# Kernel tuning notes

Hardware: AMD Instinct MI355X
Metric: run time of the kernel (lower is better)

Reference implementation:

```python
import jax, jax.numpy as jnp
import numpy as np

N_ITER = 100
EPS = 1e-12


def _corr(x, k):
    # x: [C,H,W], k: [kh,kw]; per-channel 'same' cross-correlation, zero padding
    C = x.shape[0]
    kern = jnp.broadcast_to(k, (C, 1) + k.shape)
    return jax.lax.conv_general_dilated(
        x[None], kern, window_strides=(1, 1), padding='SAME',
        feature_group_count=C,
        dimension_numbers=('NCHW', 'OIHW', 'NCHW'))[0]


def _corr_t(x, k):
    # adjoint of zero-padded 'same' correlation = correlation with flipped kernel
    return _corr(x, k[::-1, ::-1])


def _A(x, kernel, reg_kernels, w2):
    # A x = K^T K x + sum_i w_i^2 R_i^T R_i x
    out = _corr_t(_corr(x, kernel), kernel)
    for i in range(reg_kernels.shape[0]):  # small fixed number of reg kernels
        rk = reg_kernels[i]
        out = out + w2[i] * _corr_t(_corr(x, rk), rk)
    return out


def setup_inputs() -> dict:
    key = jax.random.key(0)
    k1, k2, k3, k4 = jax.random.split(key, 4)
    image = jax.random.uniform(k1, (3, 768, 768), dtype=jnp.float32)
    kernel = jax.random.uniform(k2, (15, 15), dtype=jnp.float32)
    kernel = kernel / jnp.sum(kernel)  # normalized blur PSF
    reg_kernels = jax.random.normal(k3, (2, 5, 5), dtype=jnp.float32)
    reg_kernel_weights = jax.random.uniform(
        k4, (2,), dtype=jnp.float32, minval=1e-6, maxval=1.0)
    return {'image': image, 'kernel': kernel, 'reg_kernels': reg_kernels,
            'reg_kernel_weights': reg_kernel_weights}


def reference(image, kernel, reg_kernels, reg_kernel_weights):
    w2 = reg_kernel_weights ** 2
    # CG init: x0 = image, b = image, solve A x = K^T b
    KTb = _corr_t(image, kernel)
    r0 = KTb - _A(image, kernel, reg_kernels, w2)
    xrp0 = jnp.stack([image, r0, r0])  # [3, C, H, W]: x, r, p

    def body(xrp, _):
        x, r, p = xrp[0], xrp[1], xrp[2]
        Ap = _A(p, kernel, reg_kernels, w2)
        rtr = jnp.sum(r * r, axis=(1, 2), keepdims=True)      # per-channel [C,1,1]
        ptAp = jnp.sum(p * Ap, axis=(1, 2), keepdims=True)
        alpha = rtr / (ptAp + EPS)
        x_new = x + alpha * p
        r_new = r - alpha * Ap
        beta = jnp.sum(r_new * r_new, axis=(1, 2), keepdims=True) / (rtr + EPS)
        p_new = r_new + beta * p
        return jnp.stack([x_new, r_new, p_new]), None

    xrp, _ = jax.lax.scan(jax.checkpoint(body), xrp0, None, length=N_ITER)
    return xrp
```

## Files before the change

### kernel.cpp

```cpp
#include <hip/hip_runtime.h>

#define EPS 1e-12f

constexpr int H = 768, W = 768, C = 3;
constexpr int HW = H * W;
constexpr int CHW = C * HW;

constexpr int NSLOT = 16;
constexpr int SSTR = 16;
constexpr int SCALSZ = NSLOT * SSTR;

constexpr int SPW = 100, SPH = 60;
constexpr int S0W = 84,  S0H = 46;
constexpr int S1W = 76,  S1H = 36;
constexpr int UBUF = SPH * SPW;

constexpr int IPW = 92, IPH = 60;

__device__ __forceinline__ float block_reduce_256(float v, float* redbuf) {
    #pragma unroll
    for (int off = 32; off > 0; off >>= 1) v += __shfl_down(v, off, 64);
    const int tid = threadIdx.x;
    if ((tid & 63) == 0) redbuf[tid >> 6] = v;
    __syncthreads();
    return redbuf[0] + redbuf[1] + redbuf[2] + redbuf[3];
}

__device__ __forceinline__ float sum_slots(const float* base, int c) {
    float s = 0.f;
    #pragma unroll
    for (int k = 0; k < NSLOT; ++k) s += base[k * SSTR + c];
    return s;
}

__global__ void tap_prep_k(const float* __restrict__ k15, const float* __restrict__ rks,
                           const float* __restrict__ rw, float* __restrict__ taps) {
    const int tid = threadIdx.x;
    if (tid < 240) {
        const int i = tid >> 4, j = tid & 15;
        taps[tid]       = (j < 15) ? k15[i * 15 + j] : 0.f;
        taps[240 + tid] = (j < 15) ? k15[(14 - i) * 15 + (14 - j)] : 0.f;
    }
    if (tid < 80) {
        const int kk = tid / 40, rem = tid % 40, i = rem >> 3, j = rem & 7;
        taps[480 + tid] = (j < 5) ? rks[kk * 25 + i * 5 + j] : 0.f;
        taps[560 + tid] = (j < 5) ? rks[kk * 25 + (4 - i) * 5 + (4 - j)] : 0.f;
    }
    const float w20 = rw[0] * rw[0], w21 = rw[1] * rw[1];
    for (int t = tid; t < 29 * 36; t += 256) {
        const int uy = t / 36, ux = t - uy * 36;
        float s = 0.f;
        if (ux < 29) {
            const int dy = uy - 14, dx = ux - 14;
            for (int sy = 0; sy < 15; ++sy) {
                const int ty = sy + dy;
                if ((unsigned)ty >= 15u) continue;
                for (int sx = 0; sx < 15; ++sx) {
                    const int tx = sx + dx;
                    if ((unsigned)tx < 15u) s += k15[sy * 15 + sx] * k15[ty * 15 + tx];
                }
            }
            if (dy >= -4 && dy <= 4 && dx >= -4 && dx <= 4) {
                float q0 = 0.f, q1 = 0.f;
                for (int sy = 0; sy < 5; ++sy) {
                    const int ty = sy + dy;
                    if ((unsigned)ty >= 5u) continue;
                    for (int sx = 0; sx < 5; ++sx) {
                        const int tx = sx + dx;
                        if ((unsigned)tx >= 5u) continue;
                        q0 += rks[sy * 5 + sx] * rks[ty * 5 + tx];
                        q1 += rks[25 + sy * 5 + sx] * rks[25 + ty * 5 + tx];
                    }
                }
                s += w20 * q0 + w21 * q1;
            }
        }
        taps[640 + t] = s;
    }
}

template <bool WRITEP>
__global__ __launch_bounds__(256) void interiorA_k(
    const float* __restrict__ pprev, const float* __restrict__ rvec,
    const float* __restrict__ tk,
    float* __restrict__ Ap, float* __restrict__ outP,
    const float* __restrict__ bnum, const float* __restrict__ bden,
    float* __restrict__ red)
{
    __shared__ __align__(16) float pe[IPH * IPW];
    __shared__ float redbuf[4];
    const int c = blockIdx.z;
    const int bx = 64 + blockIdx.x * 64, by = 32 + blockIdx.y * 32;
    const int tid = threadIdx.x;
    const float beta = sum_slots(bnum, c) / (sum_slots(bden, c) + EPS);
    const float* pC = pprev + c * HW;
    const float* rC = rvec + c * HW;
    const int gy0 = by - 14, gx0 = bx - 14;

    for (int t = tid; t < IPH * IPW; t += 256) {
        const int ly = t / IPW, lx = t - ly * IPW;
        const int g = (gy0 + ly) * W + gx0 + lx;
        pe[t] = fmaf(beta, pC[g], rC[g]);
    }
    __syncthreads();

    const int ox = (tid & 15) << 2;
    const int o0 = (tid >> 4) << 1;

    float a0[4], a1[4];
    #pragma unroll
    for (int k = 0; k < 4; ++k) { a0[k] = 0.f; a1[k] = 0.f; }

    {
        const float* rp = pe + o0 * IPW + ox;
        float seg[32];
        #pragma unroll
        for (int q = 0; q < 8; ++q) *(float4*)(seg + 4 * q) = *(const float4*)(rp + 4 * q);
        #pragma unroll
        for (int j = 0; j < 29; ++j) {
            const float kv = tk[j];
            #pragma unroll
            for (int k = 0; k < 4; ++k) a0[k] = fmaf(seg[j + k], kv, a0[k]);
        }
    }
    #pragma unroll 1
    for (int d = 1; d <= 28; ++d) {
        const float* rp = pe + (o0 + d) * IPW + ox;
        float seg[32];
        #pragma unroll
        for (int q = 0; q < 8; ++q) *(float4*)(seg + 4 * q) = *(const float4*)(rp + 4 * q);
        const float* kr0 = tk + d * 36;
        const float* kr1 = kr0 - 36;
        #pragma unroll
        for (int j = 0; j < 29; ++j) {
            const float kv0 = kr0[j], kv1 = kr1[j];
            #pragma unroll
            for (int k = 0; k < 4; ++k) {
                a0[k] = fmaf(seg[j + k], kv0, a0[k]);
                a1[k] = fmaf(seg[j + k], kv1, a1[k]);
            }
        }
    }
    {
        const float* rp = pe + (o0 + 29) * IPW + ox;
        float seg[32];
        #pragma unroll
        for (int q = 0; q < 8; ++q) *(float4*)(seg + 4 * q) = *(const float4*)(rp + 4 * q);
        const float* kr1 = tk + 28 * 36;
        #pragma unroll
        for (int j = 0; j < 29; ++j) {
            const float kv = kr1[j];
            #pragma unroll
            for (int k = 0; k < 4; ++k) a1[k] = fmaf(seg[j + k], kv, a1[k]);
        }
    }

    const int gbase = c * HW + (by + o0) * W + bx + ox;
    const float* c0p = pe + (o0 + 14) * IPW + ox + 14;
    const float* c1p = c0p + IPW;
    *(float4*)(Ap + gbase)     = make_float4(a0[0], a0[1], a0[2], a0[3]);
    *(float4*)(Ap + gbase + W) = make_float4(a1[0], a1[1], a1[2], a1[3]);
    float local = 0.f;
    #pragma unroll
    for (int k = 0; k < 4; ++k) local += c0p[k] * a0[k] + c1p[k] * a1[k];
    if (WRITEP) {
        *(float4*)(outP + gbase)     = make_float4(c0p[0], c0p[1], c0p[2], c0p[3]);
        *(float4*)(outP + gbase + W) = make_float4(c1p[0], c1p[1], c1p[2], c1p[3]);
    }
    const float tot = block_reduce_256(local, redbuf);
    if (tid == 0) {
        const int bid = blockIdx.y * gridDim.x + blockIdx.x;
        atomicAdd(red + (bid & (NSLOT - 1)) * SSTR + c, tot);
    }
}

template <int MODE, bool REMAP>
__global__ __launch_bounds__(256) void fusedA_k(
    const float* __restrict__ in, const float* __restrict__ rvec,
    const float* __restrict__ taps, const float* __restrict__ rw,
    float* __restrict__ Ap, float* __restrict__ outR,
    float* __restrict__ outP, float* __restrict__ outX,
    const float* __restrict__ bnum, const float* __restrict__ bden,
    float* __restrict__ red)
{
    __shared__ __align__(16) float ub[UBUF];
    __shared__ __align__(16) float st1[S1H * S1W];
    __shared__ __align__(16) float st2[S1H * S1W];
    __shared__ float redbuf[4];

    const float* kt   = taps;
    const float* ktf  = taps + 240;
    const float* rkt  = taps + 480;
    const float* rktf = taps + 560;

    int tbx, tby;
    if (REMAP) {
        const int e = blockIdx.x;
        if (e < 12)      { tbx = e;      tby = 0; }
        else if (e < 24) { tbx = e - 12; tby = 23; }
        else if (e < 46) { tbx = 0;      tby = 1 + (e - 24); }
        else             { tbx = 11;     tby = 1 + (e - 46); }
    } else { tbx = blockIdx.x; tby = blockIdx.y; }

    const int c = blockIdx.z;
    const int bx = tbx * 64, by = tby * 32;
    const int tid = threadIdx.x;
    const float* inC = in + c * HW;

    float beta = 0.f;
    if (MODE == 2) beta = sum_slots(bnum, c) / (sum_slots(bden, c) + EPS);

    for (int t = tid; t < SPH * 96; t += 256) {
        const int ly = t / 96, lx = t - ly * 96;
        const int gy = by - 14 + ly, gx = bx - 14 + lx;
        float v = 0.f;
        if ((unsigned)gy < (unsigned)H && (unsigned)gx < (unsigned)W) {
            const int g = gy * W + gx;
            v = inC[g];
            if (MODE == 2) v = rvec[c * HW + g] + beta * v;
        }
        ub[ly * SPW + lx] = v;
    }
    __syncthreads();

    const int oy = tid >> 3;
    const int ox = (tid & 7) << 3;

    {
        const int s0 = tid, s1 = tid + 256;
        const int row0 = s0 / 9, c0 = (s0 - row0 * 9) << 3;
        const int row1 = s1 / 9, c1 = (s1 - row1 * 9) << 3;
        const bool v1 = (s1 < 324);
        float b0[8], c0a[8], b1[8], c1a[8];
        #pragma unroll
        for (int k = 0; k < 8; ++k) { b0[k] = 0.f; c0a[k] = 0.f; b1[k] = 0.f; c1a[k] = 0.f; }

        float4 kb0 = *(const float4*)(rkt + 0), kb1 = *(const float4*)(rkt + 4);
        float4 kc0 = *(const float4*)(rkt + 40), kc1 = *(const float4*)(rkt + 44);
        #pragma unroll 1
        for (int i = 0; i < 5; ++i) {
            const int ip = (i < 4) ? i + 1 : 4;
            float4 nb0 = *(const float4*)(rkt + ip * 8),      nb1 = *(const float4*)(rkt + ip * 8 + 4);
            float4 nc0 = *(const float4*)(rkt + 40 + ip * 8), nc1 = *(const float4*)(rkt + 40 + ip * 8 + 4);
            float kb[8], kc[8];
            *(float4*)(kb) = kb0; *(float4*)(kb + 4) = kb1;
            *(float4*)(kc) = kc0; *(float4*)(kc + 4) = kc1;
            {
                const float* rp = ub + (row0 + 10 + i) * SPW + c0 + 8;
                float seg[16];
                #pragma unroll
                for (int q = 0; q < 4; ++q) *(float4*)(seg + 4 * q) = *(const float4*)(rp + 4 * q);
                #pragma unroll
                for (int j = 0; j < 5; ++j)
                    #pragma unroll
                    for (int k = 0; k < 8; ++k) {
                        b0[k]  = fmaf(seg[j + k + 2], kb[j], b0[k]);
                        c0a[k] = fmaf(seg[j + k + 2], kc[j], c0a[k]);
                    }
            }
            if (v1) {
                const float* rp = ub + (row1 + 10 + i) * SPW + c1 + 8;
                float seg[16];
                #pragma unroll
                for (int q = 0; q < 4; ++q) *(float4*)(seg + 4 * q) = *(const float4*)(rp + 4 * q);
                #pragma unroll
                for (int j = 0; j < 5; ++j)
                    #pragma unroll
                    for (int k = 0; k < 8; ++k) {
                        b1[k]  = fmaf(seg[j + k + 2], kb[j], b1[k]);
                        c1a[k] = fmaf(seg[j + k + 2], kc[j], c1a[k]);
                    }
            }
            kb0 = nb0; kb1 = nb1; kc0 = nc0; kc1 = nc1;
        }
        {
            const int gy = by - 2 + row0, gxb = bx - 2 + c0;
            #pragma unroll
            for (int k = 0; k < 8; ++k) {
                const bool bad = ((unsigned)gy >= (unsigned)H) || ((unsigned)(gxb + k) >= (unsigned)W);
                if (bad) { b0[k] = 0.f; c0a[k] = 0.f; }
            }
            float* o1 = st1 + row0 * S1W + c0;
            float* o2 = st2 + row0 * S1W + c0;
            *(float4*)(o1)     = make_float4(b0[0], b0[1], b0[2], b0[3]);
            *(float4*)(o1 + 4) = make_float4(b0[4], b0[5], b0[6], b0[7]);
            *(float4*)(o2)     = make_float4(c0a[0], c0a[1], c0a[2], c0a[3]);
            *(float4*)(o2 + 4) = make_float4(c0a[4], c0a[5], c0a[6], c0a[7]);
        }
        if (v1) {
            const int gy = by - 2 + row1, gxb = bx - 2 + c1;
            #pragma unroll
            for (int k = 0; k < 8; ++k) {
                const bool bad = ((unsigned)gy >= (unsigned)H) || ((unsigned)(gxb + k) >= (unsigned)W);
                if (bad) { b1[k] = 0.f; c1a[k] = 0.f; }
            }
            float* o1 = st1 + row1 * S1W + c1;
            float* o2 = st2 + row1 * S1W + c1;
            *(float4*)(o1)     = make_float4(b1[0], b1[1], b1[2], b1[3]);
            *(float4*)(o1 + 4) = make_float4(b1[4], b1[5], b1[6], b1[7]);
            *(float4*)(o2)     = make_float4(c1a[0], c1a[1], c1a[2], c1a[3]);
            *(float4*)(o2 + 4) = make_float4(c1a[4], c1a[5], c1a[6], c1a[7]);
        }
    }

    float pctr[8];
    {
        const float* ctr = ub + (oy + 14) * SPW + ox + 14;
        #pragma unroll
        for (int k = 0; k < 8; ++k) pctr[k] = ctr[k];
    }

    float vimg[8];
    if (MODE == 0) {
        #pragma unroll
        for (int k = 0; k < 8; ++k) vimg[k] = 0.f;
        #pragma unroll 1
        for (int i = 0; i < 15; ++i) {
            const float* rowp = ub + (oy + 7 + i) * SPW + ox + 4;
            float seg[28];
            #pragma unroll
            for (int q = 0; q < 7; ++q) *(float4*)(seg + 4 * q) = *(const float4*)(rowp + 4 * q);
            float kv[16];
            #pragma unroll
            for (int q = 0; q < 4; ++q) *(float4*)(kv + 4 * q) = *(const float4*)(ktf + i * 16 + 4 * q);
            #pragma unroll
            for (int j = 0; j < 15; ++j)
                #pragma unroll
                for (int k = 0; k < 8; ++k) vimg[k] = fmaf(seg[j + k + 3], kv[j], vimg[k]);
        }
    }

    const int s0 = tid, s1 = tid + 256;
    const int row0 = s0 / 10, ca0 = (s0 - row0 * 10) << 3;
    const int row1 = s1 / 10, ca1 = (s1 - row1 * 10) << 3;
    const bool av1 = (s1 < 460);
    float a0[8], a1[8];
    #pragma unroll
    for (int k = 0; k < 8; ++k) { a0[k] = 0.f; a1[k] = 0.f; }
    {
        float4 k0 = *(const float4*)(kt + 0), k1 = *(const float4*)(kt + 4);
        float4 k2 = *(const float4*)(kt + 8), k3 = *(const float4*)(kt + 12);
        #pragma unroll 1
        for (int i = 0; i < 15; ++i) {
            const int ip = (i < 14) ? i + 1 : 14;
            float4 n0 = *(const float4*)(kt + ip * 16),     n1 = *(const float4*)(kt + ip * 16 + 4);
            float4 n2 = *(const float4*)(kt + ip * 16 + 8), n3 = *(const float4*)(kt + ip * 16 + 12);
            float kv[16];
            *(float4*)(kv) = k0; *(float4*)(kv + 4) = k1;
            *(float4*)(kv + 8) = k2; *(float4*)(kv + 12) = k3;
            {
                const float* rp = ub + (row0 + i) * SPW + ca0;
                float seg[24];
                #pragma unroll
                for (int q = 0; q < 6; ++q) *(float4*)(seg + 4 * q) = *(const float4*)(rp + 4 * q);
                #pragma unroll
                for (int j = 0; j < 15; ++j)
                    #pragma unroll
                    for (int k = 0; k < 8; ++k) a0[k] = fmaf(seg[j + k], kv[j], a0[k]);
            }
            if (av1) {
                const float* rp = ub + (row1 + i) * SPW + ca1;
                float seg[24];
                #pragma unroll
                for (int q = 0; q < 6; ++q) *(float4*)(seg + 4 * q) = *(const float4*)(rp + 4 * q);
                #pragma unroll
                for (int j = 0; j < 15; ++j)
                    #pragma unroll
                    for (int k = 0; k < 8; ++k) a1[k] = fmaf(seg[j + k], kv[j], a1[k]);
            }
            k0 = n0; k1 = n1; k2 = n2; k3 = n3;
        }
    }
    {
        const int gy = by - 7 + row0, gxb = bx - 7 + ca0;
        #pragma unroll
        for (int k = 0; k < 8; ++k)
            if (((unsigned)gy >= (unsigned)H) || ((unsigned)(gxb + k) >= (unsigned)W)) a0[k] = 0.f;
    }
    if (av1) {
        const int gy = by - 7 + row1, gxb = bx - 7 + ca1;
        #pragma unroll
        for (int k = 0; k < 8; ++k)
            if (((unsigned)gy >= (unsigned)H) || ((unsigned)(gxb + k) >= (unsigned)W)) a1[k] = 0.f;
    }

    __syncthreads();

    {
        float* o = ub + row0 * S0W + ca0;
        *(float4*)(o)     = make_float4(a0[0], a0[1], a0[2], a0[3]);
        *(float4*)(o + 4) = make_float4(a0[4], a0[5], a0[6], a0[7]);
    }
    if (av1) {
        float* o = ub + row1 * S0W + ca1;
        *(float4*)(o)     = make_float4(a1[0], a1[1], a1[2], a1[3]);
        *(float4*)(o + 4) = make_float4(a1[4], a1[5], a1[6], a1[7]);
    }
    __syncthreads();

    float acc[8];
    #pragma unroll
    for (int k = 0; k < 8; ++k) acc[k] = 0.f;
    {
        float4 k0 = *(const float4*)(ktf + 0), k1 = *(const float4*)(ktf + 4);
        float4 k2 = *(const float4*)(ktf + 8), k3 = *(const float4*)(ktf + 12);
        #pragma unroll 1
        for (int i = 0; i < 15; ++i) {
            const int ip = (i < 14) ? i + 1 : 14;
            float4 n0 = *(const float4*)(ktf + ip * 16),     n1 = *(const float4*)(ktf + ip * 16 + 4);
            float4 n2 = *(const float4*)(ktf + ip * 16 + 8), n3 = *(const float4*)(ktf + ip * 16 + 12);
            float kv[16];
            *(float4*)(kv) = k0; *(float4*)(kv + 4) = k1;
            *(float4*)(kv + 8) = k2; *(float4*)(kv + 12) = k3;
            const float* rp = ub + (oy + i) * S0W + ox;
            float seg[24];
            #pragma unroll
            for (int q = 0; q < 6; ++q) *(float4*)(seg + 4 * q) = *(const float4*)(rp + 4 * q);
            #pragma unroll
            for (int j = 0; j < 15; ++j)
                #pragma unroll
                for (int k = 0; k < 8; ++k) acc[k] = fmaf(seg[j + k], kv[j], acc[k]);
            k0 = n0; k1 = n1; k2 = n2; k3 = n3;
        }
    }

    float accB[8], accC[8];
    #pragma unroll
    for (int k = 0; k < 8; ++k) { accB[k] = 0.f; accC[k] = 0.f; }
    {
        float4 kb0 = *(const float4*)(rktf + 0), kb1 = *(const float4*)(rktf + 4);
        float4 kc0 = *(const float4*)(rktf + 40), kc1 = *(const float4*)(rktf + 44);
        #pragma unroll 1
        for (int i = 0; i < 5; ++i) {
            const int ip = (i < 4) ? i + 1 : 4;
            float4 nb0 = *(const float4*)(rktf + ip * 8),      nb1 = *(const float4*)(rktf + ip * 8 + 4);
            float4 nc0 = *(const float4*)(rktf + 40 + ip * 8), nc1 = *(const float4*)(rktf + 40 + ip * 8 + 4);
            float kb[8], kc[8];
            *(float4*)(kb) = kb0; *(float4*)(kb + 4) = kb1;
            *(float4*)(kc) = kc0; *(float4*)(kc + 4) = kc1;
            const float* r1p = st1 + (oy + i) * S1W + ox;
            const float* r2p = st2 + (oy + i) * S1W + ox;
            float sA[12], sB[12];
            #pragma unroll
            for (int q = 0; q < 3; ++q) *(float4*)(sA + 4 * q) = *(const float4*)(r1p + 4 * q);
            #pragma unroll
            for (int q = 0; q < 3; ++q) *(float4*)(sB + 4 * q) = *(const float4*)(r2p + 4 * q);
            #pragma unroll
            for (int j = 0; j < 5; ++j)
                #pragma unroll
                for (int k = 0; k < 8; ++k) {
                    accB[k] = fmaf(sA[j + k], kb[j], accB[k]);
                    accC[k] = fmaf(sB[j + k], kc[j], accC[k]);
                }
            kb0 = nb0; kb1 = nb1; kc0 = nc0; kc1 = nc1;
        }
    }

    const float w0 = rw[0], w1 = rw[1];
    const float w02 = w0 * w0, w12 = w1 * w1;
    float v[8];
    #pragma unroll
    for (int k = 0; k < 8; ++k) v[k] = acc[k] + w02 * accB[k] + w12 * accC[k];

    const int g = c * HW + (by + oy) * W + bx + ox;
    float local = 0.f;
    if (MODE == 0) {
        #pragma unroll
        for (int k = 0; k < 8; ++k) v[k] = vimg[k] - v[k];
        *(float4*)(outR + g)     = make_float4(v[0], v[1], v[2], v[3]);
        *(float4*)(outR + g + 4) = make_float4(v[4], v[5], v[6], v[7]);
        *(float4*)(outP + g)     = make_float4(v[0], v[1], v[2], v[3]);
        *(float4*)(outP + g + 4) = make_float4(v[4], v[5], v[6], v[7]);
        *(float4*)(outX + g)     = make_float4(pctr[0], pctr[1], pctr[2], pctr[3]);
        *(float4*)(outX + g + 4) = make_float4(pctr[4], pctr[5], pctr[6], pctr[7]);
        #pragma unroll
        for (int k = 0; k < 8; ++k) local += v[k] * v[k];
    } else {
        *(float4*)(Ap + g)     = make_float4(v[0], v[1], v[2], v[3]);
        *(float4*)(Ap + g + 4) = make_float4(v[4], v[5], v[6], v[7]);
        #pragma unroll
        for (int k = 0; k < 8; ++k) local += pctr[k] * v[k];
        if (MODE == 2) {
            *(float4*)(outP + g)     = make_float4(pctr[0], pctr[1], pctr[2], pctr[3]);
            *(float4*)(outP + g + 4) = make_float4(pctr[4], pctr[5], pctr[6], pctr[7]);
        }
    }
    const float tot = block_reduce_256(local, redbuf);
    if (tid == 0) {
        const int bid = REMAP ? (int)blockIdx.x : (int)(blockIdx.y * gridDim.x + blockIdx.x);
        atomicAdd(red + (bid & (NSLOT - 1)) * SSTR + c, tot);
    }
}

__global__ __launch_bounds__(256) void cg_update_k(
    float* __restrict__ x, float* __restrict__ r,
    const float* __restrict__ Ap, const float* __restrict__ p,
    const float* __restrict__ rtr_cur, const float* __restrict__ ptap,
    float* __restrict__ rtr_next)
{
    __shared__ float redbuf[4];
    const int c = blockIdx.z;
    const float n = sum_slots(rtr_cur, c), d = sum_slots(ptap, c);
    const float alpha = n / (d + EPS);
    const int idx = c * HW + (blockIdx.x * 256 + threadIdx.x) * 8;
    float local = 0.f;
    #pragma unroll
    for (int h = 0; h < 2; ++h) {
        const int o = idx + 4 * h;
        float4 xv = *(float4*)(x + o);
        float4 rv = *(float4*)(r + o);
        const float4 pv = *(const float4*)(p + o);
        const float4 av = *(const float4*)(Ap + o);
        xv.x = fmaf(alpha, pv.x, xv.x); rv.x = fmaf(-alpha, av.x, rv.x);
        xv.y = fmaf(alpha, pv.y, xv.y); rv.y = fmaf(-alpha, av.y, rv.y);
        xv.z = fmaf(alpha, pv.z, xv.z); rv.z = fmaf(-alpha, av.z, rv.z);
        xv.w = fmaf(alpha, pv.w, xv.w); rv.w = fmaf(-alpha, av.w, rv.w);
        *(float4*)(x + o) = xv;
        *(float4*)(r + o) = rv;
        local += rv.x * rv.x + rv.y * rv.y + rv.z * rv.z + rv.w * rv.w;
    }
    const float tot = block_reduce_256(local, redbuf);
    if (threadIdx.x == 0)
        atomicAdd(rtr_next + ((int)blockIdx.x & (NSLOT - 1)) * SSTR + c, tot);
}

__global__ __launch_bounds__(256) void p_final_k(
    const float* __restrict__ r, const float* __restrict__ p99, float* __restrict__ pout,
    const float* __restrict__ num, const float* __restrict__ den)
{
    const int c = blockIdx.z;
    const float beta = sum_slots(num, c) / (sum_slots(den, c) + EPS);
    const int idx = c * HW + (blockIdx.x * 256 + threadIdx.x) * 8;
    #pragma unroll
    for (int h = 0; h < 2; ++h) {
        const int o = idx + 4 * h;
        const float4 rv = *(const float4*)(r + o);
        const float4 pv = *(const float4*)(p99 + o);
        *(float4*)(pout + o) = make_float4(
            fmaf(beta, pv.x, rv.x), fmaf(beta, pv.y, rv.y),
            fmaf(beta, pv.z, rv.z), fmaf(beta, pv.w, rv.w));
    }
}

extern "C" void kernel_launch(void* const* d_in, const int* in_sizes, int n_in,
                              void* d_out, int out_size, void* d_ws, size_t ws_size,
                              hipStream_t stream)
{
    const float* img = (const float*)d_in[0];
    const float* k15 = (const float*)d_in[1];
    const float* rks = (const float*)d_in[2];
    const float* rw  = (const float*)d_in[3];

    float* out = (float*)d_out;
    float* xs = out;
    float* rs = out + CHW;
    float* ps = out + 2 * CHW;

    float* ws   = (float*)d_ws;
    float* buf0 = ws;
    float* Ap   = buf0 + CHW;
    float* scal = Ap + CHW;
    float* rtr2 = scal;
    float* ptap = scal + 101 * SCALSZ;
    float* zslot = scal + 201 * SCALSZ;
    float* taps = scal + 202 * SCALSZ;

    hipMemsetAsync(scal, 0, (size_t)202 * SCALSZ * sizeof(float), stream);
    tap_prep_k<<<1, 256, 0, stream>>>(k15, rks, rw, taps);
    const float* tk = taps + 640;

    const dim3 gfull(12, 24, 3), bc(256);
    const dim3 gint(10, 22, 3), gedge(68, 1, 3);
    const dim3 ge(HW / 2048, 1, C);

    fusedA_k<0, false><<<gfull, bc, 0, stream>>>(img, nullptr, taps, rw,
                                                 nullptr, rs, buf0, xs,
                                                 nullptr, nullptr, rtr2);

    for (int i = 0; i < 100; ++i) {
        float* pin  = (i & 1) ? buf0 : ps;
        float* pcur = (i & 1) ? ps : buf0;
        if (i == 0) {
            interiorA_k<false><<<gint, bc, 0, stream>>>(buf0, buf0, tk,
                                                        Ap, nullptr, zslot, zslot, ptap);
            fusedA_k<1, true><<<gedge, bc, 0, stream>>>(buf0, nullptr, taps, rw,
                                                        Ap, nullptr, nullptr, nullptr,
                                                        nullptr, nullptr, ptap);
        } else {
            interiorA_k<true><<<gint, bc, 0, stream>>>(pin, rs, tk,
                                                       Ap, pcur,
                                                       rtr2 + i * SCALSZ, rtr2 + (i - 1) * SCALSZ,
                                                       ptap + i * SCALSZ);
            fusedA_k<2, true><<<gedge, bc, 0, stream>>>(pin, rs, taps, rw,
                                                        Ap, nullptr, pcur, nullptr,
                                                        rtr2 + i * SCALSZ, rtr2 + (i - 1) * SCALSZ,
                                                        ptap + i * SCALSZ);
        }
        cg_update_k<<<ge, bc, 0, stream>>>(xs, rs, Ap, pcur,
                                           rtr2 + i * SCALSZ, ptap + i * SCALSZ,
                                           rtr2 + (i + 1) * SCALSZ);
    }
    p_final_k<<<ge, bc, 0, stream>>>(rs, ps, ps, rtr2 + 100 * SCALSZ, rtr2 + 99 * SCALSZ);
}
```

Before: 9.706 ms.

## Merge interior and edge A-apply kernels and defer x update into next step

Merges the separate interior and edge-tile A-operator kernels into one stepA kernel with 288 blocks per channel, where the first 68 blocks handle border tiles and the rest handle the interior. The x update (x += alpha*p) moves out of the CG update kernel and into the next step's kernel, which already reads p. The CG update kernel now only updates r and its norm, and a final epilogue applies the last x update and the final p. The aim is fewer launches per iteration and less global traffic in the bandwidth-bound update kernel, at the cost of more complex per-block branching and a double-buffered p.

```diff
diff --git a/kernel.cpp b/kernel.cpp
--- a/kernel.cpp
+++ b/kernel.cpp
@@ -11,10 +11,10 @@
 constexpr int SCALSZ = NSLOT * SSTR;
 
 constexpr int SPW = 100, SPH = 60;
-constexpr int S0W = 84,  S0H = 46;
-constexpr int S1W = 76,  S1H = 36;
+constexpr int S0W = 84;
+constexpr int S1W = 76, S1H = 36;
 constexpr int UBUF = SPH * SPW;
-
+constexpr int LDSE = UBUF + 2 * S1H * S1W;
 constexpr int IPW = 92, IPH = 60;
 
 __device__ __forceinline__ float block_reduce_256(float v, float* redbuf) {
@@ -47,6 +47,7 @@
         taps[560 + tid] = (j < 5) ? rks[kk * 25 + (4 - i) * 5 + (4 - j)] : 0.f;
     }
     const float w20 = rw[0] * rw[0], w21 = rw[1] * rw[1];
+    if (tid == 0) { taps[1684] = w20; taps[1685] = w21; }
     for (int t = tid; t < 29 * 36; t += 256) {
         const int uy = t / 36, ux = t - uy * 36;
         float s = 0.f;
@@ -79,108 +80,9 @@
     }
 }
 
-template <bool WRITEP>
-__global__ __launch_bounds__(256) void interiorA_k(
-    const float* __restrict__ pprev, const float* __restrict__ rvec,
-    const float* __restrict__ tk,
-    float* __restrict__ Ap, float* __restrict__ outP,
-    const float* __restrict__ bnum, const float* __restrict__ bden,
-    float* __restrict__ red)
-{
-    __shared__ __align__(16) float pe[IPH * IPW];
-    __shared__ float redbuf[4];
-    const int c = blockIdx.z;
-    const int bx = 64 + blockIdx.x * 64, by = 32 + blockIdx.y * 32;
-    const int tid = threadIdx.x;
-    const float beta = sum_slots(bnum, c) / (sum_slots(bden, c) + EPS);
-    const float* pC = pprev + c * HW;
-    const float* rC = rvec + c * HW;
-    const int gy0 = by - 14, gx0 = bx - 14;
-
-    for (int t = tid; t < IPH * IPW; t += 256) {
-        const int ly = t / IPW, lx = t - ly * IPW;
-        const int g = (gy0 + ly) * W + gx0 + lx;
-        pe[t] = fmaf(beta, pC[g], rC[g]);
-    }
-    __syncthreads();
-
-    const int ox = (tid & 15) << 2;
-    const int o0 = (tid >> 4) << 1;
-
-    float a0[4], a1[4];
-    #pragma unroll
-    for (int k = 0; k < 4; ++k) { a0[k] = 0.f; a1[k] = 0.f; }
-
-    {
-        const float* rp = pe + o0 * IPW + ox;
-        float seg[32];
-        #pragma unroll
-        for (int q = 0; q < 8; ++q) *(float4*)(seg + 4 * q) = *(const float4*)(rp + 4 * q);
-        #pragma unroll
-        for (int j = 0; j < 29; ++j) {
-            const float kv = tk[j];
-            #pragma unroll
-            for (int k = 0; k < 4; ++k) a0[k] = fmaf(seg[j + k], kv, a0[k]);
-        }
-    }
-    #pragma unroll 1
-    for (int d = 1; d <= 28; ++d) {
-        const float* rp = pe + (o0 + d) * IPW + ox;
-        float seg[32];
-        #pragma unroll
-        for (int q = 0; q < 8; ++q) *(float4*)(seg + 4 * q) = *(const float4*)(rp + 4 * q);
-        const float* kr0 = tk + d * 36;
-        const float* kr1 = kr0 - 36;
-        #pragma unroll
-        for (int j = 0; j < 29; ++j) {
-            const float kv0 = kr0[j], kv1 = kr1[j];
-            #pragma unroll
-            for (int k = 0; k < 4; ++k) {
-                a0[k] = fmaf(seg[j + k], kv0, a0[k]);
-                a1[k] = fmaf(seg[j + k], kv1, a1[k]);
-            }
-        }
-    }
-    {
-        const float* rp = pe + (o0 + 29) * IPW + ox;
-        float seg[32];
-        #pragma unroll
-        for (int q = 0; q < 8; ++q) *(float4*)(seg + 4 * q) = *(const float4*)(rp + 4 * q);
-        const float* kr1 = tk + 28 * 36;
-        #pragma unroll
-        for (int j = 0; j < 29; ++j) {
-            const float kv = kr1[j];
-            #pragma unroll
-            for (int k = 0; k < 4; ++k) a1[k] = fmaf(seg[j + k], kv, a1[k]);
-        }
-    }
-
-    const int gbase = c * HW + (by + o0) * W + bx + ox;
-    const float* c0p = pe + (o0 + 14) * IPW + ox + 14;
-    const float* c1p = c0p + IPW;
-    *(float4*)(Ap + gbase)     = make_float4(a0[0], a0[1], a0[2], a0[3]);
-    *(float4*)(Ap + gbase + W) = make_float4(a1[0], a1[1], a1[2], a1[3]);
-    float local = 0.f;
-    #pragma unroll
-    for (int k = 0; k < 4; ++k) local += c0p[k] * a0[k] + c1p[k] * a1[k];
-    if (WRITEP) {
-        *(float4*)(outP + gbase)     = make_float4(c0p[0], c0p[1], c0p[2], c0p[3]);
-        *(float4*)(outP + gbase + W) = make_float4(c1p[0], c1p[1], c1p[2], c1p[3]);
-    }
-    const float tot = block_reduce_256(local, redbuf);
-    if (tid == 0) {
-        const int bid = blockIdx.y * gridDim.x + blockIdx.x;
-        atomicAdd(red + (bid & (NSLOT - 1)) * SSTR + c, tot);
-    }
-}
-
-template <int MODE, bool REMAP>
-__global__ __launch_bounds__(256) void fusedA_k(
-    const float* __restrict__ in, const float* __restrict__ rvec,
-    const float* __restrict__ taps, const float* __restrict__ rw,
-    float* __restrict__ Ap, float* __restrict__ outR,
-    float* __restrict__ outP, float* __restrict__ outX,
-    const float* __restrict__ bnum, const float* __restrict__ bden,
+__global__ __launch_bounds__(256) void prologue_k(
+    const float* __restrict__ img, const float* __restrict__ taps,
+    float* __restrict__ outR, float* __restrict__ outP, float* __restrict__ outX,
     float* __restrict__ red)
 {
     __shared__ __align__(16) float ub[UBUF];
@@ -192,33 +94,18 @@
     const float* ktf  = taps + 240;
     const float* rkt  = taps + 480;
     const float* rktf = taps + 560;
-
-    int tbx, tby;
-    if (REMAP) {
-        const int e = blockIdx.x;
-        if (e < 12)      { tbx = e;      tby = 0; }
-        else if (e < 24) { tbx = e - 12; tby = 23; }
-        else if (e < 46) { tbx = 0;      tby = 1 + (e - 24); }
-        else             { tbx = 11;     tby = 1 + (e - 46); }
-    } else { tbx = blockIdx.x; tby = blockIdx.y; }
+    const float w02 = taps[1684], w12 = taps[1685];
 
     const int c = blockIdx.z;
-    const int bx = tbx * 64, by = tby * 32;
+    const int bx = blockIdx.x * 64, by = blockIdx.y * 32;
     const int tid = threadIdx.x;
-    const float* inC = in + c * HW;
-
-    float beta = 0.f;
-    if (MODE == 2) beta = sum_slots(bnum, c) / (sum_slots(bden, c) + EPS);
+    const float* inC = img + c * HW;
 
     for (int t = tid; t < SPH * 96; t += 256) {
         const int ly = t / 96, lx = t - ly * 96;
         const int gy = by - 14 + ly, gx = bx - 14 + lx;
         float v = 0.f;
-        if ((unsigned)gy < (unsigned)H && (unsigned)gx < (unsigned)W) {
-            const int g = gy * W + gx;
-            v = inC[g];
-            if (MODE == 2) v = rvec[c * HW + g] + beta * v;
-        }
+        if ((unsigned)gy < (unsigned)H && (unsigned)gx < (unsigned)W) v = inC[gy * W + gx];
         ub[ly * SPW + lx] = v;
     }
     __syncthreads();
@@ -227,24 +114,21 @@
     const int ox = (tid & 7) << 3;
 
     {
-        const int s0 = tid, s1 = tid + 256;
+        const int s0 = tid, s1i = tid + 256;
         const int row0 = s0 / 9, c0 = (s0 - row0 * 9) << 3;
-        const int row1 = s1 / 9, c1 = (s1 - row1 * 9) << 3;
-        const bool v1 = (s1 < 324);
+        const int row1 = s1i / 9, c1 = (s1i - row1 * 9) << 3;
+        const bool v1 = (s1i < 324);
         float b0[8], c0a[8], b1[8], c1a[8];
         #pragma unroll
         for (int k = 0; k < 8; ++k) { b0[k] = 0.f; c0a[k] = 0.f; b1[k] = 0.f; c1a[k] = 0.f; }
-
-        float4 kb0 = *(const float4*)(rkt + 0), kb1 = *(const float4*)(rkt + 4);
-        float4 kc0 = *(const float4*)(rkt + 40), kc1 = *(const float4*)(rkt + 44);
         #pragma unroll 1
         for (int i = 0; i < 5; ++i) {
-            const int ip = (i < 4) ? i + 1 : 4;
-            float4 nb0 = *(const float4*)(rkt + ip * 8),      nb1 = *(const float4*)(rkt + ip * 8 + 4);
-            float4 nc0 = *(const float4*)(rkt + 40 + ip * 8), nc1 = *(const float4*)(rkt + 40 + ip * 8 + 4);
             float kb[8], kc[8];
-            *(float4*)(kb) = kb0; *(float4*)(kb + 4) = kb1;
-            *(float4*)(kc) = kc0; *(float4*)(kc + 4) = kc1;
+            #pragma unroll
+            for (int q = 0; q < 2; ++q) {
+                *(float4*)(kb + 4 * q) = *(const float4*)(rkt + i * 8 + 4 * q);
+                *(float4*)(kc + 4 * q) = *(const float4*)(rkt + 40 + i * 8 + 4 * q);
+            }
             {
                 const float* rp = ub + (row0 + 10 + i) * SPW + c0 + 8;
                 float seg[16];
@@ -271,34 +155,29 @@
                         c1a[k] = fmaf(seg[j + k + 2], kc[j], c1a[k]);
                     }
             }
-            kb0 = nb0; kb1 = nb1; kc0 = nc0; kc1 = nc1;
         }
         {
             const int gy = by - 2 + row0, gxb = bx - 2 + c0;
             #pragma unroll
-            for (int k = 0; k < 8; ++k) {
-                const bool bad = ((unsigned)gy >= (unsigned)H) || ((unsigned)(gxb + k) >= (unsigned)W);
-                if (bad) { b0[k] = 0.f; c0a[k] = 0.f; }
-            }
+            for (int k = 0; k < 8; ++k)
+                if (((unsigned)gy >= (unsigned)H) || ((unsigned)(gxb + k) >= (unsigned)W)) { b0[k] = 0.f; c0a[k] = 0.f; }
             float* o1 = st1 + row0 * S1W + c0;
             float* o2 = st2 + row0 * S1W + c0;
-            *(float4*)(o1)     = make_float4(b0[0], b0[1], b0[2], b0[3]);
+            *(float4*)(o1) = make_float4(b0[0], b0[1], b0[2], b0[3]);
             *(float4*)(o1 + 4) = make_float4(b0[4], b0[5], b0[6], b0[7]);
-            *(float4*)(o2)     = make_float4(c0a[0], c0a[1], c0a[2], c0a[3]);
+            *(float4*)(o2) = make_float4(c0a[0], c0a[1], c0a[2], c0a[3]);
             *(float4*)(o2 + 4) = make_float4(c0a[4], c0a[5], c0a[6], c0a[7]);
         }
         if (v1) {
             const int gy = by - 2 + row1, gxb = bx - 2 + c1;
             #pragma unroll
-            for (int k = 0; k < 8; ++k) {
-                const bool bad = ((unsigned)gy >= (unsigned)H) || ((unsigned)(gxb + k) >= (unsigned)W);
-                if (bad) { b1[k] = 0.f; c1a[k] = 0.f; }
-            }
+            for (int k = 0; k < 8; ++k)
+                if (((unsigned)gy >= (unsigned)H) || ((unsigned)(gxb + k) >= (unsigned)W)) { b1[k] = 0.f; c1a[k] = 0.f; }
             float* o1 = st1 + row1 * S1W + c1;
             float* o2 = st2 + row1 * S1W + c1;
-            *(float4*)(o1)     = make_float4(b1[0], b1[1], b1[2], b1[3]);
+            *(float4*)(o1) = make_float4(b1[0], b1[1], b1[2], b1[3]);
             *(float4*)(o1 + 4) = make_float4(b1[4], b1[5], b1[6], b1[7]);
-            *(float4*)(o2)     = make_float4(c1a[0], c1a[1], c1a[2], c1a[3]);
+            *(float4*)(o2) = make_float4(c1a[0], c1a[1], c1a[2], c1a[3]);
             *(float4*)(o2 + 4) = make_float4(c1a[4], c1a[5], c1a[6], c1a[7]);
         }
     }
@@ -311,43 +190,300 @@
     }
 
     float vimg[8];
-    if (MODE == 0) {
-        #pragma unroll
-        for (int k = 0; k < 8; ++k) vimg[k] = 0.f;
+    #pragma unroll
+    for (int k = 0; k < 8; ++k) vimg[k] = 0.f;
+    #pragma unroll 1
+    for (int i = 0; i < 15; ++i) {
+        const float* rowp = ub + (oy + 7 + i) * SPW + ox + 4;
+        float seg[28];
+        #pragma unroll
+        for (int q = 0; q < 7; ++q) *(float4*)(seg + 4 * q) = *(const float4*)(rowp + 4 * q);
+        float kv[16];
+        #pragma unroll
+        for (int q = 0; q < 4; ++q) *(float4*)(kv + 4 * q) = *(const float4*)(ktf + i * 16 + 4 * q);
+        #pragma unroll
+        for (int j = 0; j < 15; ++j)
+            #pragma unroll
+            for (int k = 0; k < 8; ++k) vimg[k] = fmaf(seg[j + k + 3], kv[j], vimg[k]);
+    }
+
+    const int s0 = tid, s1i = tid + 256;
+    const int row0 = s0 / 10, ca0 = (s0 - row0 * 10) << 3;
+    const int row1 = s1i / 10, ca1 = (s1i - row1 * 10) << 3;
+    const bool av1 = (s1i < 460);
+    float a0[8], a1[8];
+    #pragma unroll
+    for (int k = 0; k < 8; ++k) { a0[k] = 0.f; a1[k] = 0.f; }
+    #pragma unroll 1
+    for (int i = 0; i < 15; ++i) {
+        float kv[16];
+        #pragma unroll
+        for (int q = 0; q < 4; ++q) *(float4*)(kv + 4 * q) = *(const float4*)(kt + i * 16 + 4 * q);
+        {
+            const float* rp = ub + (row0 + i) * SPW + ca0;
+            float seg[24];
+            #pragma unroll
+            for (int q = 0; q < 6; ++q) *(float4*)(seg + 4 * q) = *(const float4*)(rp + 4 * q);
+            #pragma unroll
+            for (int j = 0; j < 15; ++j)
+                #pragma unroll
+                for (int k = 0; k < 8; ++k) a0[k] = fmaf(seg[j + k], kv[j], a0[k]);
+        }
+        if (av1) {
+            const float* rp = ub + (row1 + i) * SPW + ca1;
+            float seg[24];
+            #pragma unroll
+            for (int q = 0; q < 6; ++q) *(float4*)(seg + 4 * q) = *(const float4*)(rp + 4 * q);
+            #pragma unroll
+            for (int j = 0; j < 15; ++j)
+                #pragma unroll
+                for (int k = 0; k < 8; ++k) a1[k] = fmaf(seg[j + k], kv[j], a1[k]);
+        }
+    }
+    {
+        const int gy = by - 7 + row0, gxb = bx - 7 + ca0;
+        #pragma unroll
+        for (int k = 0; k < 8; ++k)
+            if (((unsigned)gy >= (unsigned)H) || ((unsigned)(gxb + k) >= (unsigned)W)) a0[k] = 0.f;
+    }
+    if (av1) {
+        const int gy = by - 7 + row1, gxb = bx - 7 + ca1;
+        #pragma unroll
+        for (int k = 0; k < 8; ++k)
+            if (((unsigned)gy >= (unsigned)H) || ((unsigned)(gxb + k) >= (unsigned)W)) a1[k] = 0.f;
+    }
+    __syncthreads();
+    {
+        float* o = ub + row0 * S0W + ca0;
+        *(float4*)(o) = make_float4(a0[0], a0[1], a0[2], a0[3]);
+        *(float4*)(o + 4) = make_float4(a0[4], a0[5], a0[6], a0[7]);
+    }
+    if (av1) {
+        float* o = ub + row1 * S0W + ca1;
+        *(float4*)(o) = make_float4(a1[0], a1[1], a1[2], a1[3]);
+        *(float4*)(o + 4) = make_float4(a1[4], a1[5], a1[6], a1[7]);
+    }
+    __syncthreads();
+
+    float acc[8];
+    #pragma unroll
+    for (int k = 0; k < 8; ++k) acc[k] = 0.f;
+    #pragma unroll 1
+    for (int i = 0; i < 15; ++i) {
+        float kv[16];
+        #pragma unroll
+        for (int q = 0; q < 4; ++q) *(float4*)(kv + 4 * q) = *(const float4*)(ktf + i * 16 + 4 * q);
+        const float* rp = ub + (oy + i) * S0W + ox;
+        float seg[24];
+        #pragma unroll
+        for (int q = 0; q < 6; ++q) *(float4*)(seg + 4 * q) = *(const float4*)(rp + 4 * q);
+        #pragma unroll
+        for (int j = 0; j < 15; ++j)
+            #pragma unroll
+            for (int k = 0; k < 8; ++k) acc[k] = fmaf(seg[j + k], kv[j], acc[k]);
+    }
+    float accB[8], accC[8];
+    #pragma unroll
+    for (int k = 0; k < 8; ++k) { accB[k] = 0.f; accC[k] = 0.f; }
+    #pragma unroll 1
+    for (int i = 0; i < 5; ++i) {
+        float kb[8], kc[8];
+        #pragma unroll
+        for (int q = 0; q < 2; ++q) {
+            *(float4*)(kb + 4 * q) = *(const float4*)(rktf + i * 8 + 4 * q);
+            *(float4*)(kc + 4 * q) = *(const float4*)(rktf + 40 + i * 8 + 4 * q);
+        }
+        const float* r1p = st1 + (oy + i) * S1W + ox;
+        const float* r2p = st2 + (oy + i) * S1W + ox;
+        float sA[12], sB[12];
+        #pragma unroll
+        for (int q = 0; q < 3; ++q) *(float4*)(sA + 4 * q) = *(const float4*)(r1p + 4 * q);
+        #pragma unroll
+        for (int q = 0; q < 3; ++q) *(float4*)(sB + 4 * q) = *(const float4*)(r2p + 4 * q);
+        #pragma unroll
+        for (int j = 0; j < 5; ++j)
+            #pragma unroll
+            for (int k = 0; k < 8; ++k) {
+                accB[k] = fmaf(sA[j + k], kb[j], accB[k]);
+                accC[k] = fmaf(sB[j + k], kc[j], accC[k]);
+            }
+    }
+
+    float v[8];
+    #pragma unroll
+    for (int k = 0; k < 8; ++k) v[k] = vimg[k] - (acc[k] + w02 * accB[k] + w12 * accC[k]);
+
+    const int g = c * HW + (by + oy) * W + bx + ox;
+    *(float4*)(outR + g)     = make_float4(v[0], v[1], v[2], v[3]);
+    *(float4*)(outR + g + 4) = make_float4(v[4], v[5], v[6], v[7]);
+    *(float4*)(outP + g)     = make_float4(v[0], v[1], v[2], v[3]);
+    *(float4*)(outP + g + 4) = make_float4(v[4], v[5], v[6], v[7]);
+    *(float4*)(outX + g)     = make_float4(pctr[0], pctr[1], pctr[2], pctr[3]);
+    *(float4*)(outX + g + 4) = make_float4(pctr[4], pctr[5], pctr[6], pctr[7]);
+    float local = 0.f;
+    #pragma unroll
+    for (int k = 0; k < 8; ++k) local += v[k] * v[k];
+    const float tot = block_reduce_256(local, redbuf);
+    if (tid == 0) {
+        const int bid = blockIdx.y * gridDim.x + blockIdx.x;
+        atomicAdd(red + (bid & (NSLOT - 1)) * SSTR + c, tot);
+    }
+}
+
+template <bool FIRST>
+__global__ __launch_bounds__(256) void stepA_k(
+    const float* __restrict__ pold, const float* __restrict__ rvec,
+    float* __restrict__ x, const float* __restrict__ taps,
+    float* __restrict__ Apnew, float* __restrict__ pnew,
+    const float* __restrict__ rtrI, const float* __restrict__ rtrIm1,
+    const float* __restrict__ ptapIm1, float* __restrict__ ptapI)
+{
+    __shared__ __align__(16) float lds[LDSE];
+    __shared__ float redbuf[4];
+    const int c = blockIdx.z;
+    const int tid = threadIdx.x;
+    const int bid = blockIdx.x;
+
+    float alpha = 0.f, beta = 0.f;
+    if (!FIRST) {
+        const float ri   = sum_slots(rtrI, c);
+        const float rim1 = sum_slots(rtrIm1, c);
+        const float ptm1 = sum_slots(ptapIm1, c);
+        beta  = ri / (rim1 + EPS);
+        alpha = rim1 / (ptm1 + EPS);
+    }
+
+    float S1 = 0.f;
+
+    if (bid < 68) {
+        float* ub  = lds;
+        float* st1 = lds + UBUF;
+        float* st2 = st1 + S1H * S1W;
+        const float* kt   = taps;
+        const float* ktf  = taps + 240;
+        const float* rkt  = taps + 480;
+        const float* rktf = taps + 560;
+        const float w02 = taps[1684], w12 = taps[1685];
+
+        int tbx, tby;
+        { const int e = bid;
+          if (e < 12)      { tbx = e;      tby = 0; }
+          else if (e < 24) { tbx = e - 12; tby = 23; }
+          else if (e < 46) { tbx = 0;      tby = 1 + (e - 24); }
+          else             { tbx = 11;     tby = 1 + (e - 46); } }
+        const int bx = tbx * 64, by = tby * 32;
+
+        for (int s = tid; s < SPH * 96; s += 256) {
+            const int ly = s / 96, lx = s - ly * 96;
+            const int gy = by - 14 + ly, gx = bx - 14 + lx;
+            float pe = 0.f;
+            if ((unsigned)gy < (unsigned)H && (unsigned)gx < (unsigned)W) {
+                const int g = c * HW + gy * W + gx;
+                const float pv = pold[g];
+                if (FIRST) pe = pv;
+                else {
+                    pe = fmaf(beta, pv, rvec[g]);
+                    if (ly >= 14 && ly < 46 && lx >= 14 && lx < 78) {
+                        pnew[g] = pe;
+                        x[g] = fmaf(alpha, pv, x[g]);
+                    }
+                }
+            }
+            ub[ly * SPW + lx] = pe;
+        }
+        __syncthreads();
+
+        const int oy = tid >> 3;
+        const int ox = (tid & 7) << 3;
+
+        {
+            const int s0 = tid, s1i = tid + 256;
+            const int row0 = s0 / 9, c0 = (s0 - row0 * 9) << 3;
+            const int row1 = s1i / 9, c1 = (s1i - row1 * 9) << 3;
+            const bool v1 = (s1i < 324);
+            float b0[8], c0a[8], b1[8], c1a[8];
+            #pragma unroll
+            for (int k = 0; k < 8; ++k) { b0[k] = 0.f; c0a[k] = 0.f; b1[k] = 0.f; c1a[k] = 0.f; }
+            #pragma unroll 1
+            for (int i = 0; i < 5; ++i) {
+                float kb[8], kc[8];
+                #pragma unroll
+                for (int q = 0; q < 2; ++q) {
+                    *(float4*)(kb + 4 * q) = *(const float4*)(rkt + i * 8 + 4 * q);
+                    *(float4*)(kc + 4 * q) = *(const float4*)(rkt + 40 + i * 8 + 4 * q);
+                }
+                {
+                    const float* rp = ub + (row0 + 10 + i) * SPW + c0 + 8;
+                    float seg[16];
+                    #pragma unroll
+                    for (int q = 0; q < 4; ++q) *(float4*)(seg + 4 * q) = *(const float4*)(rp + 4 * q);
+                    #pragma unroll
+                    for (int j = 0; j < 5; ++j)
+                        #pragma unroll
+                        for (int k = 0; k < 8; ++k) {
+                            b0[k]  = fmaf(seg[j + k + 2], kb[j], b0[k]);
+                            c0a[k] = fmaf(seg[j + k + 2], kc[j], c0a[k]);
+                        }
+                }
+                if (v1) {
+                    const float* rp = ub + (row1 + 10 + i) * SPW + c1 + 8;
+                    float seg[16];
+                    #pragma unroll
+                    for (int q = 0; q < 4; ++q) *(float4*)(seg + 4 * q) = *(const float4*)(rp + 4 * q);
+                    #pragma unroll
+                    for (int j = 0; j < 5; ++j)
+                        #pragma unroll
+                        for (int k = 0; k < 8; ++k) {
+                            b1[k]  = fmaf(seg[j + k + 2], kb[j], b1[k]);
+                            c1a[k] = fmaf(seg[j + k + 2], kc[j], c1a[k]);
+                        }
+                }
+            }
+            {
+                const int gy = by - 2 + row0, gxb = bx - 2 + c0;
+                #pragma unroll
+                for (int k = 0; k < 8; ++k)
+                    if (((unsigned)gy >= (unsigned)H) || ((unsigned)(gxb + k) >= (unsigned)W)) { b0[k] = 0.f; c0a[k] = 0.f; }
+                float* o1 = st1 + row0 * S1W + c0;
+                float* o2 = st2 + row0 * S1W + c0;
+                *(float4*)(o1) = make_float4(b0[0], b0[1], b0[2], b0[3]);
+                *(float4*)(o1 + 4) = make_float4(b0[4], b0[5], b0[6], b0[7]);
+                *(float4*)(o2) = make_float4(c0a[0], c0a[1], c0a[2], c0a[3]);
+                *(float4*)(o2 + 4) = make_float4(c0a[4], c0a[5], c0a[6], c0a[7]);
+            }
+            if (v1) {
+                const int gy = by - 2 + row1, gxb = bx - 2 + c1;
+                #pragma unroll
+                for (int k = 0; k < 8; ++k)
+                    if (((unsigned)gy >= (unsigned)H) || ((unsigned)(gxb + k) >= (unsigned)W)) { b1[k] = 0.f; c1a[k] = 0.f; }
+                float* o1 = st1 + row1 * S1W + c1;
+                float* o2 = st2 + row1 * S1W + c1;
+                *(float4*)(o1) = make_float4(b1[0], b1[1], b1[2], b1[3]);
+                *(float4*)(o1 + 4) = make_float4(b1[4], b1[5], b1[6], b1[7]);
+                *(float4*)(o2) = make_float4(c1a[0], c1a[1], c1a[2], c1a[3]);
+                *(float4*)(o2 + 4) = make_float4(c1a[4], c1a[5], c1a[6], c1a[7]);
+            }
+        }
+
+        float pctr[8];
+        {
+            const float* ctr = ub + (oy + 14) * SPW + ox + 14;
+            #pragma unroll
+            for (int k = 0; k < 8; ++k) pctr[k] = ctr[k];
+        }
+
+        const int s0 = tid, s1i = tid + 256;
+        const int row0 = s0 / 10, ca0 = (s0 - row0 * 10) << 3;
+        const int row1 = s1i / 10, ca1 = (s1i - row1 * 10) << 3;
+        const bool av1 = (s1i < 460);
+        float a0[8], a1[8];
+        #pragma unroll
+        for (int k = 0; k < 8; ++k) { a0[k] = 0.f; a1[k] = 0.f; }
         #pragma unroll 1
         for (int i = 0; i < 15; ++i) {
-            const float* rowp = ub + (oy + 7 + i) * SPW + ox + 4;
-            float seg[28];
-            #pragma unroll
-            for (int q = 0; q < 7; ++q) *(float4*)(seg + 4 * q) = *(const float4*)(rowp + 4 * q);
             float kv[16];
             #pragma unroll
-            for (int q = 0; q < 4; ++q) *(float4*)(kv + 4 * q) = *(const float4*)(ktf + i * 16 + 4 * q);
-            #pragma unroll
-            for (int j = 0; j < 15; ++j)
-                #pragma unroll
-                for (int k = 0; k < 8; ++k) vimg[k] = fmaf(seg[j + k + 3], kv[j], vimg[k]);
-        }
-    }
-
-    const int s0 = tid, s1 = tid + 256;
-    const int row0 = s0 / 10, ca0 = (s0 - row0 * 10) << 3;
-    const int row1 = s1 / 10, ca1 = (s1 - row1 * 10) << 3;
-    const bool av1 = (s1 < 460);
-    float a0[8], a1[8];
-    #pragma unroll
-    for (int k = 0; k < 8; ++k) { a0[k] = 0.f; a1[k] = 0.f; }
-    {
-        float4 k0 = *(const float4*)(kt + 0), k1 = *(const float4*)(kt + 4);
-        float4 k2 = *(const float4*)(kt + 8), k3 = *(const float4*)(kt + 12);
-        #pragma unroll 1
-        for (int i = 0; i < 15; ++i) {
-            const int ip = (i < 14) ? i + 1 : 14;
-            float4 n0 = *(const float4*)(kt + ip * 16),     n1 = *(const float4*)(kt + ip * 16 + 4);
-            float4 n2 = *(const float4*)(kt + ip * 16 + 8), n3 = *(const float4*)(kt + ip * 16 + 12);
-            float kv[16];
-            *(float4*)(kv) = k0; *(float4*)(kv + 4) = k1;
-            *(float4*)(kv + 8) = k2; *(float4*)(kv + 12) = k3;
+            for (int q = 0; q < 4; ++q) *(float4*)(kv + 4 * q) = *(const float4*)(kt + i * 16 + 4 * q);
             {
                 const float* rp = ub + (row0 + i) * SPW + ca0;
                 float seg[24];
@@ -368,50 +504,40 @@
                     #pragma unroll
                     for (int k = 0; k < 8; ++k) a1[k] = fmaf(seg[j + k], kv[j], a1[k]);
             }
-            k0 = n0; k1 = n1; k2 = n2; k3 = n3;
-        }
-    }
-    {
-        const int gy = by - 7 + row0, gxb = bx - 7 + ca0;
-        #pragma unroll
-        for (int k = 0; k < 8; ++k)
-            if (((unsigned)gy >= (unsigned)H) || ((unsigned)(gxb + k) >= (unsigned)W)) a0[k] = 0.f;
-    }
-    if (av1) {
-        const int gy = by - 7 + row1, gxb = bx - 7 + ca1;
-        #pragma unroll
-        for (int k = 0; k < 8; ++k)
-            if (((unsigned)gy >= (unsigned)H) || ((unsigned)(gxb + k) >= (unsigned)W)) a1[k] = 0.f;
-    }
-
-    __syncthreads();
-
-    {
-        float* o = ub + row0 * S0W + ca0;
-        *(float4*)(o)     = make_float4(a0[0], a0[1], a0[2], a0[3]);
-        *(float4*)(o + 4) = make_float4(a0[4], a0[5], a0[6], a0[7]);
-    }
-    if (av1) {
-        float* o = ub + row1 * S0W + ca1;
-        *(float4*)(o)     = make_float4(a1[0], a1[1], a1[2], a1[3]);
-        *(float4*)(o + 4) = make_float4(a1[4], a1[5], a1[6], a1[7]);
-    }
-    __syncthreads();
-
-    float acc[8];
-    #pragma unroll
-    for (int k = 0; k < 8; ++k) acc[k] = 0.f;
-    {
-        float4 k0 = *(const float4*)(ktf + 0), k1 = *(const float4*)(ktf + 4);
-        float4 k2 = *(const float4*)(ktf + 8), k3 = *(const float4*)(ktf + 12);
+        }
+        {
+            const int gy = by - 7 + row0, gxb = bx - 7 + ca0;
+            #pragma unroll
+            for (int k = 0; k < 8; ++k)
+                if (((unsigned)gy >= (unsigned)H) || ((unsigned)(gxb + k) >= (unsigned)W)) a0[k] = 0.f;
+        }
+        if (av1) {
+            const int gy = by - 7 + row1, gxb = bx - 7 + ca1;
+            #pragma unroll
+            for (int k = 0; k < 8; ++k)
+                if (((unsigned)gy >= (unsigned)H) || ((unsigned)(gxb + k) >= (unsigned)W)) a1[k] = 0.f;
+        }
+        __syncthreads();
+        {
+            float* o = ub + row0 * S0W + ca0;
+            *(float4*)(o) = make_float4(a0[0], a0[1], a0[2], a0[3]);
+            *(float4*)(o + 4) = make_float4(a0[4], a0[5], a0[6], a0[7]);
+        }
+        if (av1) {
+            float* o = ub + row1 * S0W + ca1;
+            *(float4*)(o) = make_float4(a1[0], a1[1], a1[2], a1[3]);
+            *(float4*)(o + 4) = make_float4(a1[4], a1[5], a1[6], a1[7]);
+        }
+        __syncthreads();
+
+        float acc[8];
+        #pragma unroll
+        for (int k = 0; k < 8; ++k) acc[k] = 0.f;
         #pragma unroll 1
         for (int i = 0; i < 15; ++i) {
-            const int ip = (i < 14) ? i + 1 : 14;
-            float4 n0 = *(const float4*)(ktf + ip * 16),     n1 = *(const float4*)(ktf + ip * 16 + 4);
-            float4 n2 = *(const float4*)(ktf + ip * 16 + 8), n3 = *(const float4*)(ktf + ip * 16 + 12);
             float kv[16];
-            *(float4*)(kv) = k0; *(float4*)(kv + 4) = k1;
-            *(float4*)(kv + 8) = k2; *(float4*)(kv + 12) = k3;
+            #pragma unroll
+            for (int q = 0; q < 4; ++q) *(float4*)(kv + 4 * q) = *(const float4*)(ktf + i * 16 + 4 * q);
             const float* rp = ub + (oy + i) * S0W + ox;
             float seg[24];
             #pragma unroll
@@ -420,24 +546,18 @@
             for (int j = 0; j < 15; ++j)
                 #pragma unroll
                 for (int k = 0; k < 8; ++k) acc[k] = fmaf(seg[j + k], kv[j], acc[k]);
-            k0 = n0; k1 = n1; k2 = n2; k3 = n3;
-        }
-    }
-
-    float accB[8], accC[8];
-    #pragma unroll
-    for (int k = 0; k < 8; ++k) { accB[k] = 0.f; accC[k] = 0.f; }
-    {
-        float4 kb0 = *(const float4*)(rktf + 0), kb1 = *(const float4*)(rktf + 4);
-        float4 kc0 = *(const float4*)(rktf + 40), kc1 = *(const float4*)(rktf + 44);
+        }
+        float accB[8], accC[8];
+        #pragma unroll
+        for (int k = 0; k < 8; ++k) { accB[k] = 0.f; accC[k] = 0.f; }
         #pragma unroll 1
         for (int i = 0; i < 5; ++i) {
-            const int ip = (i < 4) ? i + 1 : 4;
-            float4 nb0 = *(const float4*)(rktf + ip * 8),      nb1 = *(const float4*)(rktf + ip * 8 + 4);
-            float4 nc0 = *(const float4*)(rktf + 40 + ip * 8), nc1 = *(const float4*)(rktf + 40 + ip * 8 + 4);
             float kb[8], kc[8];
-            *(float4*)(kb) = kb0; *(float4*)(kb + 4) = kb1;
-            *(float4*)(kc) = kc0; *(float4*)(kc + 4) = kc1;
+            #pragma unroll
+            for (int q = 0; q < 2; ++q) {
+                *(float4*)(kb + 4 * q) = *(const float4*)(rktf + i * 8 + 4 * q);
+                *(float4*)(kc + 4 * q) = *(const float4*)(rktf + 40 + i * 8 + 4 * q);
+            }
             const float* r1p = st1 + (oy + i) * S1W + ox;
             const float* r2p = st2 + (oy + i) * S1W + ox;
             float sA[12], sB[12];
@@ -452,90 +572,150 @@
                     accB[k] = fmaf(sA[j + k], kb[j], accB[k]);
                     accC[k] = fmaf(sB[j + k], kc[j], accC[k]);
                 }
-            kb0 = nb0; kb1 = nb1; kc0 = nc0; kc1 = nc1;
-        }
-    }
-
-    const float w0 = rw[0], w1 = rw[1];
-    const float w02 = w0 * w0, w12 = w1 * w1;
-    float v[8];
-    #pragma unroll
-    for (int k = 0; k < 8; ++k) v[k] = acc[k] + w02 * accB[k] + w12 * accC[k];
-
-    const int g = c * HW + (by + oy) * W + bx + ox;
-    float local = 0.f;
-    if (MODE == 0) {
-        #pragma unroll
-        for (int k = 0; k < 8; ++k) v[k] = vimg[k] - v[k];
-        *(float4*)(outR + g)     = make_float4(v[0], v[1], v[2], v[3]);
-        *(float4*)(outR + g + 4) = make_float4(v[4], v[5], v[6], v[7]);
-        *(float4*)(outP + g)     = make_float4(v[0], v[1], v[2], v[3]);
-        *(float4*)(outP + g + 4) = make_float4(v[4], v[5], v[6], v[7]);
-        *(float4*)(outX + g)     = make_float4(pctr[0], pctr[1], pctr[2], pctr[3]);
-        *(float4*)(outX + g + 4) = make_float4(pctr[4], pctr[5], pctr[6], pctr[7]);
-        #pragma unroll
-        for (int k = 0; k < 8; ++k) local += v[k] * v[k];
+        }
+
+        float v[8];
+        #pragma unroll
+        for (int k = 0; k < 8; ++k) v[k] = acc[k] + w02 * accB[k] + w12 * accC[k];
+
+        const int g = c * HW + (by + oy) * W + bx + ox;
+        *(float4*)(Apnew + g)     = make_float4(v[0], v[1], v[2], v[3]);
+        *(float4*)(Apnew + g + 4) = make_float4(v[4], v[5], v[6], v[7]);
+        #pragma unroll
+        for (int k = 0; k < 8; ++k) S1 += pctr[k] * v[k];
     } else {
-        *(float4*)(Ap + g)     = make_float4(v[0], v[1], v[2], v[3]);
-        *(float4*)(Ap + g + 4) = make_float4(v[4], v[5], v[6], v[7]);
-        #pragma unroll
-        for (int k = 0; k < 8; ++k) local += pctr[k] * v[k];
-        if (MODE == 2) {
-            *(float4*)(outP + g)     = make_float4(pctr[0], pctr[1], pctr[2], pctr[3]);
-            *(float4*)(outP + g + 4) = make_float4(pctr[4], pctr[5], pctr[6], pctr[7]);
-        }
-    }
-    const float tot = block_reduce_256(local, redbuf);
-    if (tid == 0) {
-        const int bid = REMAP ? (int)blockIdx.x : (int)(blockIdx.y * gridDim.x + blockIdx.x);
-        atomicAdd(red + (bid & (NSLOT - 1)) * SSTR + c, tot);
-    }
+        const float* tk = taps + 640;
+        const int b = bid - 68;
+        const int bx = 64 + (b % 10) * 64, by = 32 + (b / 10) * 32;
+        const int gy0 = by - 14, gx0 = bx - 14;
+
+        for (int s = tid; s < IPH * IPW; s += 256) {
+            const int ly = s / IPW, lx = s - ly * IPW;
+            const int g = c * HW + (gy0 + ly) * W + (gx0 + lx);
+            const float pv = pold[g];
+            float pe;
+            if (FIRST) pe = pv;
+            else {
+                pe = fmaf(beta, pv, rvec[g]);
+                if (ly >= 14 && ly < 46 && lx >= 14 && lx < 78) {
+                    pnew[g] = pe;
+                    x[g] = fmaf(alpha, pv, x[g]);
+                }
+            }
+            lds[s] = pe;
+        }
+        __syncthreads();
+
+        const int ox = (tid & 15) << 2;
+        const int o0 = (tid >> 4) << 1;
+
+        float a0[4], a1[4];
+        #pragma unroll
+        for (int k = 0; k < 4; ++k) { a0[k] = 0.f; a1[k] = 0.f; }
+        {
+            const float* rp = lds + o0 * IPW + ox;
+            float seg[32];
+            #pragma unroll
+            for (int q = 0; q < 8; ++q) *(float4*)(seg + 4 * q) = *(const float4*)(rp + 4 * q);
+            #pragma unroll
+            for (int j = 0; j < 29; ++j) {
+                const float kv = tk[j];
+                #pragma unroll
+                for (int k = 0; k < 4; ++k) a0[k] = fmaf(seg[j + k], kv, a0[k]);
+            }
+        }
+        #pragma unroll 1
+        for (int d = 1; d <= 28; ++d) {
+            const float* rp = lds + (o0 + d) * IPW + ox;
+            float seg[32];
+            #pragma unroll
+            for (int q = 0; q < 8; ++q) *(float4*)(seg + 4 * q) = *(const float4*)(rp + 4 * q);
+            const float* kr0 = tk + d * 36;
+            const float* kr1 = kr0 - 36;
+            #pragma unroll
+            for (int j = 0; j < 29; ++j) {
+                const float kv0 = kr0[j], kv1 = kr1[j];
+                #pragma unroll
+                for (int k = 0; k < 4; ++k) {
+                    a0[k] = fmaf(seg[j + k], kv0, a0[k]);
+                    a1[k] = fmaf(seg[j + k], kv1, a1[k]);
+                }
+            }
+        }
+        {
+            const float* rp = lds + (o0 + 29) * IPW + ox;
+            float seg[32];
+            #pragma unroll
+            for (int q = 0; q < 8; ++q) *(float4*)(seg + 4 * q) = *(const float4*)(rp + 4 * q);
+            const float* kr1 = tk + 28 * 36;
+            #pragma unroll
+            for (int j = 0; j < 29; ++j) {
+                const float kv = kr1[j];
+                #pragma unroll
+                for (int k = 0; k < 4; ++k) a1[k] = fmaf(seg[j + k], kv, a1[k]);
+            }
+        }
+
+        const int gbase = c * HW + (by + o0) * W + bx + ox;
+        const float* c0p = lds + (o0 + 14) * IPW + ox + 14;
+        const float* c1p = c0p + IPW;
+        *(float4*)(Apnew + gbase)     = make_float4(a0[0], a0[1], a0[2], a0[3]);
+        *(float4*)(Apnew + gbase + W) = make_float4(a1[0], a1[1], a1[2], a1[3]);
+        #pragma unroll
+        for (int k = 0; k < 4; ++k) S1 += c0p[k] * a0[k] + c1p[k] * a1[k];
+    }
+
+    const float tot = block_reduce_256(S1, redbuf);
+    if (tid == 0) atomicAdd(ptapI + (bid & (NSLOT - 1)) * SSTR + c, tot);
 }
 
-__global__ __launch_bounds__(256) void cg_update_k(
-    float* __restrict__ x, float* __restrict__ r,
-    const float* __restrict__ Ap, const float* __restrict__ p,
-    const float* __restrict__ rtr_cur, const float* __restrict__ ptap,
-    float* __restrict__ rtr_next)
+__global__ __launch_bounds__(256) void cgr_k(
+    float* __restrict__ r, const float* __restrict__ Ap,
+    const float* __restrict__ rtrI, const float* __restrict__ ptapI,
+    float* __restrict__ rtrNext)
 {
     __shared__ float redbuf[4];
     const int c = blockIdx.z;
-    const float n = sum_slots(rtr_cur, c), d = sum_slots(ptap, c);
-    const float alpha = n / (d + EPS);
+    const float alpha = sum_slots(rtrI, c) / (sum_slots(ptapI, c) + EPS);
     const int idx = c * HW + (blockIdx.x * 256 + threadIdx.x) * 8;
     float local = 0.f;
     #pragma unroll
     for (int h = 0; h < 2; ++h) {
         const int o = idx + 4 * h;
-        float4 xv = *(float4*)(x + o);
         float4 rv = *(float4*)(r + o);
-        const float4 pv = *(const float4*)(p + o);
         const float4 av = *(const float4*)(Ap + o);
-        xv.x = fmaf(alpha, pv.x, xv.x); rv.x = fmaf(-alpha, av.x, rv.x);
-        xv.y = fmaf(alpha, pv.y, xv.y); rv.y = fmaf(-alpha, av.y, rv.y);
-        xv.z = fmaf(alpha, pv.z, xv.z); rv.z = fmaf(-alpha, av.z, rv.z);
-        xv.w = fmaf(alpha, pv.w, xv.w); rv.w = fmaf(-alpha, av.w, rv.w);
-        *(float4*)(x + o) = xv;
+        rv.x = fmaf(-alpha, av.x, rv.x);
+        rv.y = fmaf(-alpha, av.y, rv.y);
+        rv.z = fmaf(-alpha, av.z, rv.z);
+        rv.w = fmaf(-alpha, av.w, rv.w);
         *(float4*)(r + o) = rv;
         local += rv.x * rv.x + rv.y * rv.y + rv.z * rv.z + rv.w * rv.w;
     }
     const float tot = block_reduce_256(local, redbuf);
     if (threadIdx.x == 0)
-        atomicAdd(rtr_next + ((int)blockIdx.x & (NSLOT - 1)) * SSTR + c, tot);
+        atomicAdd(rtrNext + ((int)blockIdx.x & (NSLOT - 1)) * SSTR + c, tot);
 }
 
-__global__ __launch_bounds__(256) void p_final_k(
-    const float* __restrict__ r, const float* __restrict__ p99, float* __restrict__ pout,
-    const float* __restrict__ num, const float* __restrict__ den)
+__global__ __launch_bounds__(256) void ep_k(
+    float* __restrict__ x, const float* __restrict__ r100, const float* __restrict__ p99,
+    float* __restrict__ pout,
+    const float* __restrict__ rtr99s, const float* __restrict__ rtr100s,
+    const float* __restrict__ ptap99s)
 {
     const int c = blockIdx.z;
-    const float beta = sum_slots(num, c) / (sum_slots(den, c) + EPS);
+    const float rtr99 = sum_slots(rtr99s, c);
+    const float alpha = rtr99 / (sum_slots(ptap99s, c) + EPS);
+    const float beta  = sum_slots(rtr100s, c) / (rtr99 + EPS);
     const int idx = c * HW + (blockIdx.x * 256 + threadIdx.x) * 8;
     #pragma unroll
     for (int h = 0; h < 2; ++h) {
         const int o = idx + 4 * h;
-        const float4 rv = *(const float4*)(r + o);
         const float4 pv = *(const float4*)(p99 + o);
+        const float4 rv = *(const float4*)(r100 + o);
+        float4 xv = *(float4*)(x + o);
+        xv.x = fmaf(alpha, pv.x, xv.x); xv.y = fmaf(alpha, pv.y, xv.y);
+        xv.z = fmaf(alpha, pv.z, xv.z); xv.w = fmaf(alpha, pv.w, xv.w);
+        *(float4*)(x + o) = xv;
         *(float4*)(pout + o) = make_float4(
             fmaf(beta, pv.x, rv.x), fmaf(beta, pv.y, rv.y),
             fmaf(beta, pv.z, rv.z), fmaf(beta, pv.w, rv.w));
@@ -556,49 +736,40 @@
     float* rs = out + CHW;
     float* ps = out + 2 * CHW;
 
-    float* ws   = (float*)d_ws;
-    float* buf0 = ws;
-    float* Ap   = buf0 + CHW;
-    float* scal = Ap + CHW;
-    float* rtr2 = scal;
-    float* ptap = scal + 101 * SCALSZ;
-    float* zslot = scal + 201 * SCALSZ;
-    float* taps = scal + 202 * SCALSZ;
-
-    hipMemsetAsync(scal, 0, (size_t)202 * SCALSZ * sizeof(float), stream);
+    float* ws = (float*)d_ws;
+    float* pA   = ws;
+    float* pB   = ws + CHW;
+    float* Ap   = ws + 2 * CHW;
+    float* scal = ws + 3 * CHW;
+    float* rtrS  = scal;
+    float* ptapS = scal + 101 * SCALSZ;
+    float* taps  = scal + 201 * SCALSZ;
+
+    float* pbuf[2] = { pA, pB };
+
+    hipMemsetAsync(scal, 0, (size_t)201 * SCALSZ * sizeof(float), stream);
     tap_prep_k<<<1, 256, 0, stream>>>(k15, rks, rw, taps);
-    const float* tk = taps + 640;
-
-    const dim3 gfull(12, 24, 3), bc(256);
-    const dim3 gint(10, 22, 3), gedge(68, 1, 3);
-    const dim3 ge(HW / 2048, 1, C);
-
-    fusedA_k<0, false><<<gfull, bc, 0, stream>>>(img, nullptr, taps, rw,
-                                                 nullptr, rs, buf0, xs,
-                                                 nullptr, nullptr, rtr2);
+
+    const dim3 bc(256);
+    prologue_k<<<dim3(12, 24, 3), bc, 0, stream>>>(img, taps, rs, pA, xs, rtrS);
 
     for (int i = 0; i < 100; ++i) {
-        float* pin  = (i & 1) ? buf0 : ps;
-        float* pcur = (i & 1) ? ps : buf0;
         if (i == 0) {
-            interiorA_k<false><<<gint, bc, 0, stream>>>(buf0, buf0, tk,
-                                                        Ap, nullptr, zslot, zslot, ptap);
-            fusedA_k<1, true><<<gedge, bc, 0, stream>>>(buf0, nullptr, taps, rw,
-                                                        Ap, nullptr, nullptr, nullptr,
-                                                        nullptr, nullptr, ptap);
+            stepA_k<true><<<dim3(288, 1, 3), bc, 0, stream>>>(
+                pA, rs, xs, taps, Ap, nullptr,
+                rtrS, rtrS, ptapS, ptapS);
         } else {
-            interiorA_k<true><<<gint, bc, 0, stream>>>(pin, rs, tk,
-                                                       Ap, pcur,
-                                                       rtr2 + i * SCALSZ, rtr2 + (i - 1) * SCALSZ,
-                                                       ptap + i * SCALSZ);
-            fusedA_k<2, true><<<gedge, bc, 0, stream>>>(pin, rs, taps, rw,
-                                                        Ap, nullptr, pcur, nullptr,
-                                                        rtr2 + i * SCALSZ, rtr2 + (i - 1) * SCALSZ,
-                                                        ptap + i * SCALSZ);
-        }
-        cg_update_k<<<ge, bc, 0, stream>>>(xs, rs, Ap, pcur,
-                                           rtr2 + i * SCALSZ, ptap + i * SCALSZ,
-                                           rtr2 + (i + 1) * SCALSZ);
-    }
-    p_final_k<<<ge, bc, 0, stream>>>(rs, ps, ps, rtr2 + 100 * SCALSZ, rtr2 + 99 * SCALSZ);
+            stepA_k<false><<<dim3(288, 1, 3), bc, 0, stream>>>(
+                pbuf[(i - 1) & 1], rs, xs, taps, Ap, pbuf[i & 1],
+                rtrS + (size_t)i * SCALSZ, rtrS + (size_t)(i - 1) * SCALSZ,
+                ptapS + (size_t)(i - 1) * SCALSZ, ptapS + (size_t)i * SCALSZ);
+        }
+        cgr_k<<<dim3(288, 1, 3), bc, 0, stream>>>(
+            rs, Ap, rtrS + (size_t)i * SCALSZ, ptapS + (size_t)i * SCALSZ,
+            rtrS + (size_t)(i + 1) * SCALSZ);
+    }
+    ep_k<<<dim3(288, 1, 3), bc, 0, stream>>>(
+        xs, rs, pB, ps,
+        rtrS + (size_t)99 * SCALSZ, rtrS + (size_t)100 * SCALSZ,
+        ptapS + (size_t)99 * SCALSZ);
 }
```

Measured after the change: 8.744 ms. -9.9%, faster.
